# Kernel optimization log

Hardware: AMD Instinct MI355X
Metric: run time of the kernel (lower is better)

## Reference

```python
import jax, jax.numpy as jnp
import numpy as np

B, S, V, D, H, L, FF = 2, 1024, 32000, 512, 8, 4, 2048
DK = D // H
WIN, GLOB = 128, 16
EPS = 1e-5


def setup_inputs() -> dict:
    key = jax.random.key(0)
    ks = jax.random.split(key, 12)
    def rn(k, shape, s=0.02):
        return jax.random.normal(k, shape, jnp.float32) * s
    ln2 = jnp.stack([jnp.ones((L, 2, D)), jnp.zeros((L, 2, D))], axis=2)   # [L, 2 norms, (scale,bias), D]
    ln3 = jnp.stack([jnp.ones((L, 3, D)), jnp.zeros((L, 3, D))], axis=2)   # [L, 3 norms, (scale,bias), D]
    fln = jnp.stack([jnp.ones((D,)), jnp.zeros((D,))], axis=0)             # [(scale,bias), D]
    return {
        "src": jax.random.randint(ks[0], (B, S), 0, V),
        "tgt": jax.random.randint(ks[1], (B, S), 0, V),
        "enc_embed": rn(ks[2], (V, D)),
        "dec_embed": rn(ks[3], (V, D)),
        "enc_attn_w": rn(ks[4], (L, 4, D, D)),   # q,k,v,o projections
        "enc_attn_b": jnp.zeros((L, 4, D)),
        "enc_ln": ln2,
        "enc_ffn_w1": rn(ks[5], (L, D, FF)),
        "enc_ffn_b1": jnp.zeros((L, FF)),
        "enc_ffn_w2": rn(ks[6], (L, FF, D)),
        "enc_ffn_b2": jnp.zeros((L, D)),
        "enc_final_ln": fln,
        "dec_attn_w": rn(ks[7], (L, 8, D, D)),   # self q,k,v,o then cross q,k,v,o
        "dec_attn_b": jnp.zeros((L, 8, D)),
        "dec_ln": ln3,
        "dec_ffn_w1": rn(ks[8], (L, D, FF)),
        "dec_ffn_b1": jnp.zeros((L, FF)),
        "dec_ffn_w2": rn(ks[9], (L, FF, D)),
        "dec_ffn_b2": jnp.zeros((L, D)),
        "dec_final_ln": fln,
        "out_w": rn(ks[10], (D, V)),
        "out_b": jnp.zeros((V,)),
    }


def _ln(x, p):
    m = jnp.mean(x, -1, keepdims=True)
    v = jnp.var(x, -1, keepdims=True)
    return p[0] * (x - m) * jax.lax.rsqrt(v + EPS) + p[1]


def _rope(x):
    # x: [B, H, S, DK]; half-split rotary embedding
    half = DK // 2
    pos = jnp.arange(x.shape[2], dtype=jnp.float32)
    inv = 1.0 / (10000.0 ** (jnp.arange(half, dtype=jnp.float32) / half))
    ang = pos[:, None] * inv[None, :]                   # [S, half]
    c, s = jnp.cos(ang), jnp.sin(ang)
    x1, x2 = x[..., :half], x[..., half:]
    return jnp.concatenate([x1 * c - x2 * s, x1 * s + x2 * c], axis=-1)


def _mask(n, causal):
    # local sliding window + global tokens, optional causal
    i = jnp.arange(n)[:, None]
    j = jnp.arange(n)[None, :]
    allowed = jnp.abs(i - j) <= WIN
    allowed = allowed | (i < GLOB) | (j < GLOB)
    if causal:
        allowed = allowed & (j <= i)
    return allowed


def _attn(q_in, k_in, v_in, w, b, causal):
    # w: [4, D, D] (q,k,v,o), b: [4, D]
    def heads(x, idx):
        y = x @ w[idx] + b[idx]
        return y.reshape(x.shape[0], x.shape[1], H, DK).transpose(0, 2, 1, 3)  # [B,H,S,DK]
    Q, K, Vh = heads(q_in, 0), heads(k_in, 1), heads(v_in, 2)
    Q, K = _rope(Q), _rope(K)
    scores = jnp.einsum('bhqd,bhkd->bhqk', Q, K) / np.sqrt(DK).astype(np.float32)
    scores = jnp.where(_mask(q_in.shape[1], causal)[None, None], scores, -1e9)
    A = jax.nn.softmax(scores, axis=-1)
    o = jnp.einsum('bhqk,bhkd->bhqd', A, Vh).transpose(0, 2, 1, 3).reshape(q_in.shape[0], q_in.shape[1], D)
    return o @ w[3] + b[3]


def _ffn(x, w1, b1, w2, b2):
    return jax.nn.gelu(x @ w1 + b1) @ w2 + b2


def _forward(src, tgt, enc_embed, dec_embed, enc_attn_w, enc_attn_b, enc_ln,
             enc_ffn_w1, enc_ffn_b1, enc_ffn_w2, enc_ffn_b2, enc_final_ln,
             dec_attn_w, dec_attn_b, dec_ln, dec_ffn_w1, dec_ffn_b1,
             dec_ffn_w2, dec_ffn_b2, dec_final_ln, out_w, out_b):
    sqrt_d = np.sqrt(D).astype(np.float32)
    # encoder
    x = enc_embed[src] * sqrt_d
    for l in range(L):
        n = _ln(x, enc_ln[l, 0])
        x = x + _attn(n, n, n, enc_attn_w[l], enc_attn_b[l], False)
        n = _ln(x, enc_ln[l, 1])
        x = x + _ffn(n, enc_ffn_w1[l], enc_ffn_b1[l], enc_ffn_w2[l], enc_ffn_b2[l])
    mem = _ln(x, enc_final_ln)
    # decoder
    y = dec_embed[tgt] * sqrt_d
    for l in range(L):
        n = _ln(y, dec_ln[l, 0])
        y = y + _attn(n, n, n, dec_attn_w[l, :4], dec_attn_b[l, :4], True)
        n = _ln(y, dec_ln[l, 1])
        y = y + _attn(n, mem, mem, dec_attn_w[l, 4:], dec_attn_b[l, 4:], False)
        n = _ln(y, dec_ln[l, 2])
        y = y + _ffn(n, dec_ffn_w1[l], dec_ffn_b1[l], dec_ffn_w2[l], dec_ffn_b2[l])
    y = _ln(y, dec_final_ln)
    return y @ out_w + out_b


def reference(src, tgt, enc_embed, dec_embed, enc_attn_w, enc_attn_b, enc_ln,
              enc_ffn_w1, enc_ffn_b1, enc_ffn_w2, enc_ffn_b2, enc_final_ln,
              dec_attn_w, dec_attn_b, dec_ln, dec_ffn_w1, dec_ffn_b1,
              dec_ffn_w2, dec_ffn_b2, dec_final_ln, out_w, out_b):
    return _forward(src, tgt, enc_embed, dec_embed, enc_attn_w, enc_attn_b, enc_ln,
                    enc_ffn_w1, enc_ffn_b1, enc_ffn_w2, enc_ffn_b2, enc_final_ln,
                    dec_attn_w, dec_attn_b, dec_ln, dec_ffn_w1, dec_ffn_b1,
                    dec_ffn_w2, dec_ffn_b2, dec_final_ln, out_w, out_b)
```

## Files before the change

kernel.cpp:

```cpp
#include <hip/hip_runtime.h>
#include <cstdint>
#include <cstddef>

#define S_LEN 1024
#define DM 512
#define NHEAD 8
#define HDIM 64
#define NLAYER 4
#define FFD 2048
#define VOC 32000
#define WINSZ 128
#define GLOBSZ 16

using half8 = __attribute__((ext_vector_type(8))) _Float16;
using f32x4 = __attribute__((ext_vector_type(4))) float;

static __device__ __forceinline__ f32x4 mfma16(half8 a, half8 b, f32x4 c) {
  return __builtin_amdgcn_mfma_f32_16x16x32_f16(a, b, c, 0, 0, 0);
}

typedef __attribute__((address_space(1))) const void gvoid;
typedef __attribute__((address_space(3))) void lvoid;
static __device__ __forceinline__ void gload16(const void* g, void* l) {
  __builtin_amdgcn_global_load_lds((gvoid*)g, (lvoid*)l, 16, 0, 0);
}
template <int N>
static __device__ __forceinline__ void waitv() {
  asm volatile("s_waitcnt vmcnt(%0)" :: "i"(N) : "memory");
}

__global__ __launch_bounds__(256) void transpose2_k(const float* __restrict__ inA,
                                                    const float* __restrict__ inB,
                                                    _Float16* __restrict__ outA,
                                                    _Float16* __restrict__ outB,
                                                    int R, int C, int splitZ)
{
  __shared__ float t[32][33];
  int z = blockIdx.z;
  const float* ip;
  _Float16* op;
  if (z < splitZ) { ip = inA + (size_t)z * R * C; op = outA + (size_t)z * R * C; }
  else { ip = inB + (size_t)(z - splitZ) * R * C; op = outB + (size_t)(z - splitZ) * R * C; }
  int c0 = blockIdx.x * 32, r0 = blockIdx.y * 32;
  int tx = threadIdx.x & 31, ty = threadIdx.x >> 5;
#pragma unroll
  for (int i = 0; i < 32; i += 8)
    t[ty + i][tx] = ip[(size_t)(r0 + ty + i) * C + c0 + tx];
  __syncthreads();
#pragma unroll
  for (int i = 0; i < 32; i += 8)
    op[(size_t)(c0 + ty + i) * R + r0 + tx] = (_Float16)t[tx][ty + i];
}

__global__ __launch_bounds__(256) void embed2_k(const int* __restrict__ src,
                                                const int* __restrict__ tgt,
                                                const float* __restrict__ enc_embed,
                                                const float* __restrict__ dec_embed,
                                                const float* __restrict__ enc_ln0,
                                                const float* __restrict__ dec_ln0,
                                                float* __restrict__ xbuf,
                                                float* __restrict__ ybuf,
                                                _Float16* __restrict__ nbuf,
                                                _Float16* __restrict__ nbuf2)
{
  int which = blockIdx.y;
  const int* ids = which ? tgt : src;
  const float* emb = which ? dec_embed : enc_embed;
  const float* gamma = which ? dec_ln0 : enc_ln0;
  const float* beta = gamma + 512;
  float* xout = which ? ybuf : xbuf;
  _Float16* nout = which ? nbuf2 : nbuf;

  int row = blockIdx.x * 4 + (threadIdx.x >> 6);
  int lane = threadIdx.x & 63;
  const float* er = emb + (size_t)ids[row] * DM + lane * 8;
  float4 v0 = *(const float4*)er;
  float4 v1 = *(const float4*)(er + 4);
  float vals[8] = {v0.x, v0.y, v0.z, v0.w, v1.x, v1.y, v1.z, v1.w};
  float s = 0.f, ss = 0.f;
#pragma unroll
  for (int j = 0; j < 8; ++j) {
    vals[j] *= 22.627416997969522f;
    s += vals[j]; ss += vals[j] * vals[j];
  }
#pragma unroll
  for (int m = 1; m < 64; m <<= 1) { s += __shfl_xor(s, m); ss += __shfl_xor(ss, m); }
  float mean = s * (1.f / 512.f);
  float var = ss * (1.f / 512.f) - mean * mean;
  float rstd = rsqrtf(var + 1e-5f);
  float* xr = xout + (size_t)row * DM + lane * 8;
  _Float16* orow = nout + (size_t)row * DM + lane * 8;
  const float* gp = gamma + lane * 8;
  const float* bp = beta + lane * 8;
#pragma unroll
  for (int j = 0; j < 8; ++j) {
    xr[j] = vals[j];
    orow[j] = (_Float16)(gp[j] * (vals[j] - mean) * rstd + bp[j]);
  }
}

__global__ __launch_bounds__(256) void ln_k(const float* __restrict__ x,
                                            const float* __restrict__ gamma,
                                            const float* __restrict__ beta,
                                            _Float16* __restrict__ outp)
{
  int row = blockIdx.x * 4 + (threadIdx.x >> 6);
  int lane = threadIdx.x & 63;
  const float* xr = x + (size_t)row * DM + lane * 8;
  float4 v0 = *(const float4*)xr;
  float4 v1 = *(const float4*)(xr + 4);
  float vals[8] = {v0.x, v0.y, v0.z, v0.w, v1.x, v1.y, v1.z, v1.w};
  float s = 0.f, ss = 0.f;
#pragma unroll
  for (int j = 0; j < 8; ++j) { s += vals[j]; ss += vals[j] * vals[j]; }
#pragma unroll
  for (int m = 1; m < 64; m <<= 1) { s += __shfl_xor(s, m); ss += __shfl_xor(ss, m); }
  float mean = s * (1.f / 512.f);
  float var = ss * (1.f / 512.f) - mean * mean;
  float rstd = rsqrtf(var + 1e-5f);
  _Float16* orow = outp + (size_t)row * DM + lane * 8;
  const float* gp = gamma + lane * 8;
  const float* bp = beta + lane * 8;
#pragma unroll
  for (int j = 0; j < 8; ++j)
    orow[j] = (_Float16)(gp[j] * (vals[j] - mean) * rstd + bp[j]);
}

template <int BM, int BN, int EPI, int MODE, bool SWZ = false, bool NT = false, int PIPE = 3>
__global__ __launch_bounds__(256) void gemm_k(const _Float16* __restrict__ A,
                                              const _Float16* __restrict__ B,
                                              const float* __restrict__ bias,
                                              const float* __restrict__ resid,
                                              void* __restrict__ Cout,
                                              _Float16* __restrict__ vtout,
                                              int M, int N, int K)
{
  constexpr bool WIDE = (BN >= 64);
  constexpr int WAVE_M = WIDE ? BM / 4 : BM / 2;
  constexpr int WAVE_N = WIDE ? BN : BN / 2;
  constexpr int FMW = WAVE_M / 16;
  constexpr int FNW = WIDE ? BN / 16 : BN / 32;
  constexpr int LPS = BM / 32 + BN / 32;
  static_assert(MODE == 0 || (WIDE && BN == 64), "rope modes need 64-col waves");

  __shared__ __align__(16) _Float16 As[PIPE][BM * 64];
  __shared__ __align__(16) _Float16 Bs[PIPE][BN * 64];
  const int tid = threadIdx.x;
  const int lane = tid & 63, wid = tid >> 6;
  const int g = lane >> 4, ql = lane & 15;

  int bm, bn;
  if constexpr (SWZ) {
    const int gx = gridDim.x;
    const int nwg = gx * gridDim.y;
    const int orig = blockIdx.y * gx + blockIdx.x;
    const int q = nwg >> 3, r = nwg & 7;
    const int xcd = orig & 7, rest = orig >> 3;
    const int id = (xcd < r ? xcd * (q + 1) : r * (q + 1) + (xcd - r) * q) + rest;
    bm = (id % gx) * BM; bn = (id / gx) * BN;
  } else {
    bm = blockIdx.x * BM; bn = blockIdx.y * BN;
  }
  const int wm = WIDE ? wid * WAVE_M : (wid >> 1) * WAVE_M;
  const int wn = WIDE ? 0 : (wid & 1) * WAVE_N;

  const _Float16* Bp;
  if constexpr (MODE == 2) {
    int srcrow0 = ((bn >> 10) * 8 + 5 + ((bn >> 9) & 1)) * 512 + (bn & 511);
    Bp = B + (size_t)srcrow0 * K;
  } else {
    Bp = B + (size_t)bn * K;
  }

  f32x4 acc[FMW][FNW];
#pragma unroll
  for (int a = 0; a < FMW; ++a)
#pragma unroll
    for (int b = 0; b < FNW; ++b) acc[a][b] = f32x4{0.f, 0.f, 0.f, 0.f};

  auto stage = [&](int buf, int kt) {
#pragma unroll
    for (int r2 = 0; r2 < BM / 32; ++r2) {
      int off = r2 * 4096 + tid * 16;
      int row = off >> 7, slot = (off >> 4) & 7;
      gload16(A + (size_t)(bm + row) * K + kt + ((slot ^ (row & 7)) << 3),
              (char*)&As[buf][0] + r2 * 4096 + wid * 1024);
    }
#pragma unroll
    for (int r2 = 0; r2 < BN / 32; ++r2) {
      int off = r2 * 4096 + tid * 16;
      int row = off >> 7, slot = (off >> 4) & 7;
      gload16(Bp + (size_t)row * K + kt + ((slot ^ (row & 7)) << 3),
              (char*)&Bs[buf][0] + r2 * 4096 + wid * 1024);
    }
  };

  auto compute = [&](int cur) {
#pragma unroll
    for (int kk = 0; kk < 2; ++kk) {
      half8 af[FMW], bf[FNW];
#pragma unroll
      for (int a = 0; a < FMW; ++a) {
        int row = wm + a * 16 + ql;
        af[a] = *(const half8*)((const char*)&As[cur][0] + row * 128 + (((kk * 4 + g) ^ (row & 7)) << 4));
      }
#pragma unroll
      for (int b = 0; b < FNW; ++b) {
        int row = wn + b * 16 + ql;
        bf[b] = *(const half8*)((const char*)&Bs[cur][0] + row * 128 + (((kk * 4 + g) ^ (row & 7)) << 4));
      }
#pragma unroll
      for (int a = 0; a < FMW; ++a)
#pragma unroll
        for (int b = 0; b < FNW; ++b) acc[a][b] = mfma16(af[a], bf[b], acc[a][b]);
    }
  };

  const int nk = K >> 6;
  stage(0, 0);
  stage(1, 64);
  if constexpr (PIPE == 4) stage(2, 128);
  for (int t = 0; t < nk; ++t) {
    if constexpr (PIPE == 3) {
      if (t + 1 < nk) waitv<LPS>(); else waitv<0>();
    } else {
      if (t + 2 < nk) waitv<2 * LPS>();
      else if (t + 1 < nk) waitv<LPS>();
      else waitv<0>();
    }
    __builtin_amdgcn_s_barrier();
    __builtin_amdgcn_sched_barrier(0);
    compute(t % PIPE);
    if (t + PIPE - 1 < nk) stage((t + PIPE - 1) % PIPE, (t + PIPE - 1) << 6);
  }

#pragma unroll
  for (int a = 0; a < FMW; ++a) {
    const int row0 = bm + wm + a * 16 + g * 4;
    float v[FNW][4];
#pragma unroll
    for (int b2 = 0; b2 < FNW; ++b2) {
      int col = bn + wn + b2 * 16 + ql;
      float bv;
      if constexpr (MODE == 2) {
        int bcol = ((col >> 10) * 8 + 5 + ((col >> 9) & 1)) * 512 + (col & 511);
        bv = bias[bcol];
      } else {
        bv = bias[col];
      }
#pragma unroll
      for (int r2 = 0; r2 < 4; ++r2) v[b2][r2] = acc[a][b2][r2] + bv;
    }
    if constexpr (MODE != 0) {
      const int seg = bn >> 9;
      bool dorope = (MODE == 3) || (MODE == 1 && seg < 2) ||
                    (MODE == 2 && ((bn >> 9) & 1) == 0);
      if (dorope) {
        const float scale = (MODE == 3 || (MODE == 1 && seg == 0)) ? 0.125f : 1.0f;
#pragma unroll
        for (int b2 = 0; b2 < 2; ++b2) {
          int d = b2 * 16 + ql;
          float inv = __expf(-(float)d * 0.28782313662425574f);
#pragma unroll
          for (int r2 = 0; r2 < 4; ++r2) {
            float sp = (float)((row0 & 1023) + r2);
            float sn, cs; __sincosf(sp * inv, &sn, &cs);
            float x1 = v[b2][r2], x2 = v[b2 + 2][r2];
            v[b2][r2]     = (x1 * cs - x2 * sn) * scale;
            v[b2 + 2][r2] = (x1 * sn + x2 * cs) * scale;
          }
        }
      }
    }
#pragma unroll
    for (int b2 = 0; b2 < FNW; ++b2) {
      int col = bn + wn + b2 * 16 + ql;
      if constexpr (MODE == 1) {
        if (col < 1024) {
#pragma unroll
          for (int r2 = 0; r2 < 4; ++r2)
            ((_Float16*)Cout)[(size_t)(row0 + r2) * 1024 + col] = (_Float16)v[b2][r2];
        } else {
          int rowidx = ((row0 >> 10) << 9) + (col - 1024);
          union { _Float16 h[4]; uint2 u; } pk;
#pragma unroll
          for (int r2 = 0; r2 < 4; ++r2) pk.h[r2] = (_Float16)v[b2][r2];
          *(uint2*)&vtout[((size_t)rowidx << 10) + (row0 & 1023)] = pk.u;
        }
      } else if constexpr (MODE == 2) {
        if ((col & 1023) < 512) {
#pragma unroll
          for (int r2 = 0; r2 < 4; ++r2)
            ((_Float16*)Cout)[(size_t)(row0 + r2) * 2048 + ((col >> 10) << 9) + (col & 511)] = (_Float16)v[b2][r2];
        } else {
          int rowidx = (col & ~1023) + ((row0 >> 10) << 9) + (col & 511);
          union { _Float16 h[4]; uint2 u; } pk;
#pragma unroll
          for (int r2 = 0; r2 < 4; ++r2) pk.h[r2] = (_Float16)v[b2][r2];
          *(uint2*)&vtout[((size_t)rowidx << 10) + (row0 & 1023)] = pk.u;
        }
      } else {
#pragma unroll
        for (int r2 = 0; r2 < 4; ++r2) {
          float x = v[b2][r2];
          if constexpr (EPI == 1) {
            float u = x;
            x = u / (1.f + __expf(-1.5957691216057308f * (u + 0.044715f * u * u * u)));
          }
          if constexpr (EPI == 2) x += resid[(size_t)(row0 + r2) * N + col];
          if constexpr (EPI == 0 || EPI == 1)
            ((_Float16*)Cout)[(size_t)(row0 + r2) * N + col] = (_Float16)x;
          else if constexpr (NT)
            __builtin_nontemporal_store(x, &((float*)Cout)[(size_t)(row0 + r2) * N + col]);
          else
            ((float*)Cout)[(size_t)(row0 + r2) * N + col] = x;
        }
      }
    }
  }
}

__global__ __launch_bounds__(256) void gemmlg_k(const _Float16* __restrict__ A,
                                                const _Float16* __restrict__ B,
                                                const float* __restrict__ bias,
                                                float* __restrict__ Cout,
                                                int N, int K)
{
  __shared__ __align__(16) _Float16 As[2][128 * 64];
  __shared__ __align__(16) _Float16 Bs[2][128 * 64];
  const int tid = threadIdx.x;
  const int lane = tid & 63, wid = tid >> 6;
  const int g = lane >> 4, ql = lane & 15;

  const int gx = gridDim.x;
  const int nwg = gx * gridDim.y;
  const int orig = blockIdx.y * gx + blockIdx.x;
  const int q = nwg >> 3, r = nwg & 7;
  const int xcd = orig & 7, rest = orig >> 3;
  const int id = (xcd < r ? xcd * (q + 1) : r * (q + 1) + (xcd - r) * q) + rest;
  const int bm = (id % gx) * 128, bn = (id / gx) * 128;
  const int wm = (wid >> 1) * 64, wn = (wid & 1) * 64;

  const _Float16* Bp = B + (size_t)bn * K;

  f32x4 acc[4][4];
#pragma unroll
  for (int a = 0; a < 4; ++a)
#pragma unroll
    for (int b = 0; b < 4; ++b) acc[a][b] = f32x4{0.f, 0.f, 0.f, 0.f};

  auto stage = [&](int buf, int kt) {
#pragma unroll
    for (int r2 = 0; r2 < 4; ++r2) {
      int off = r2 * 4096 + tid * 16;
      int row = off >> 7, slot = (off >> 4) & 7;
      gload16(A + (size_t)(bm + row) * K + kt + ((slot ^ (row & 7)) << 3),
              (char*)&As[buf][0] + r2 * 4096 + wid * 1024);
    }
#pragma unroll
    for (int r2 = 0; r2 < 4; ++r2) {
      int off = r2 * 4096 + tid * 16;
      int row = off >> 7, slot = (off >> 4) & 7;
      gload16(Bp + (size_t)row * K + kt + ((slot ^ (row & 7)) << 3),
              (char*)&Bs[buf][0] + r2 * 4096 + wid * 1024);
    }
  };

  const int nk = K >> 6;
  stage(0, 0);
  for (int t = 0; t < nk; ++t) {
    waitv<0>();
    __builtin_amdgcn_s_barrier();
    __builtin_amdgcn_sched_barrier(0);
    if (t + 1 < nk) stage((t + 1) & 1, (t + 1) << 6);
    const int cur = t & 1;
#pragma unroll
    for (int kk = 0; kk < 2; ++kk) {
      half8 af[4], bf[4];
#pragma unroll
      for (int a = 0; a < 4; ++a) {
        int row = wm + a * 16 + ql;
        af[a] = *(const half8*)((const char*)&As[cur][0] + row * 128 + (((kk * 4 + g) ^ (row & 7)) << 4));
      }
#pragma unroll
      for (int b = 0; b < 4; ++b) {
        int row = wn + b * 16 + ql;
        bf[b] = *(const half8*)((const char*)&Bs[cur][0] + row * 128 + (((kk * 4 + g) ^ (row & 7)) << 4));
      }
#pragma unroll
      for (int a = 0; a < 4; ++a)
#pragma unroll
        for (int b = 0; b < 4; ++b) acc[a][b] = mfma16(af[a], bf[b], acc[a][b]);
    }
  }

#pragma unroll
  for (int a = 0; a < 4; ++a) {
    const int row0 = bm + wm + a * 16 + g * 4;
#pragma unroll
    for (int b2 = 0; b2 < 4; ++b2) {
      int col = bn + wn + b2 * 16 + ql;
      float bv = bias[col];
#pragma unroll
      for (int r2 = 0; r2 < 4; ++r2)
        __builtin_nontemporal_store(acc[a][b2][r2] + bv,
                                    &Cout[(size_t)(row0 + r2) * N + col]);
    }
  }
}

template <bool CAUSAL>
__global__ __launch_bounds__(128) void attn_k(const _Float16* __restrict__ qb, int qs, int qoff,
                                              const _Float16* __restrict__ kb, int ks, int koff,
                                              const _Float16* __restrict__ vt,
                                              _Float16* __restrict__ out)
{
  __shared__ _Float16 plds[2][16 * 40];
  const int bh = blockIdx.y, b = bh >> 3, h = bh & 7;
  const int wid = threadIdx.x >> 6, lane = threadIdx.x & 63;
  const int g = lane >> 4, ql = lane & 15;
  const int q0 = blockIdx.x * 32 + wid * 16;
  const size_t rb = (size_t)b * S_LEN;

  half8 qf0, qf1;
  {
    const _Float16* qp = qb + (rb + q0 + ql) * qs + qoff + h * HDIM + g * 8;
    qf0 = *(const half8*)qp;
    qf1 = *(const half8*)(qp + 32);
  }
  float mrun[4] = {-1e30f, -1e30f, -1e30f, -1e30f};
  float srun[4] = {0.f, 0.f, 0.f, 0.f};
  f32x4 oacc[4];
#pragma unroll
  for (int c = 0; c < 4; ++c) oacc[c] = f32x4{0.f, 0.f, 0.f, 0.f};

  const _Float16* vbase = vt + (((size_t)(b * 512 + h * HDIM)) << 10);
  _Float16* pw = plds[wid];

  auto proc = [&](int k0) {
    const _Float16* kp = kb + (rb + k0 + ql) * ks + koff + h * HDIM + g * 8;
    half8 kf00 = *(const half8*)kp;
    half8 kf01 = *(const half8*)(kp + 32);
    half8 kf10 = *(const half8*)(kp + (size_t)16 * ks);
    half8 kf11 = *(const half8*)(kp + (size_t)16 * ks + 32);

    f32x4 s0 = f32x4{0.f, 0.f, 0.f, 0.f};
    f32x4 s1 = f32x4{0.f, 0.f, 0.f, 0.f};
    s0 = mfma16(qf0, kf00, s0); s0 = mfma16(qf1, kf01, s0);
    s1 = mfma16(qf0, kf10, s1); s1 = mfma16(qf1, kf11, s1);

    float p0[4], p1[4];
#pragma unroll
    for (int r = 0; r < 4; ++r) {
      int i = q0 + 4 * g + r;
      int j0 = k0 + ql, j1 = j0 + 16;
      float a0 = s0[r], a1 = s1[r];
      int d0 = i - j0, d1 = i - j1;
      bool ok0 = (d0 <= WINSZ && d0 >= -WINSZ) || (i < GLOBSZ) || (j0 < GLOBSZ);
      bool ok1 = (d1 <= WINSZ && d1 >= -WINSZ) || (i < GLOBSZ) || (j1 < GLOBSZ);
      if (CAUSAL) { ok0 = ok0 && (j0 <= i); ok1 = ok1 && (j1 <= i); }
      a0 = ok0 ? a0 : -1e9f;
      a1 = ok1 ? a1 : -1e9f;
      float mx = fmaxf(a0, a1);
      mx = fmaxf(mx, __shfl_xor(mx, 1));
      mx = fmaxf(mx, __shfl_xor(mx, 2));
      mx = fmaxf(mx, __shfl_xor(mx, 4));
      mx = fmaxf(mx, __shfl_xor(mx, 8));
      float mnew = fmaxf(mrun[r], mx);
      float alpha = __expf(mrun[r] - mnew);
      float e0 = __expf(a0 - mnew), e1 = __expf(a1 - mnew);
      float ps = e0 + e1;
      ps += __shfl_xor(ps, 1);
      ps += __shfl_xor(ps, 2);
      ps += __shfl_xor(ps, 4);
      ps += __shfl_xor(ps, 8);
      srun[r] = srun[r] * alpha + ps;
      mrun[r] = mnew;
#pragma unroll
      for (int c = 0; c < 4; ++c) oacc[c][r] *= alpha;
      p0[r] = e0; p1[r] = e1;
    }
#pragma unroll
    for (int r = 0; r < 4; ++r) {
      pw[(4 * g + r) * 40 + ql] = (_Float16)p0[r];
      pw[(4 * g + r) * 40 + 16 + ql] = (_Float16)p1[r];
    }
    half8 pa = *(const half8*)&pw[ql * 40 + g * 8];
#pragma unroll
    for (int c = 0; c < 4; ++c) {
      half8 vf = *(const half8*)(vbase + (((size_t)(16 * c + ql)) << 10) + k0 + 8 * g);
      oacc[c] = mfma16(pa, vf, oacc[c]);
    }
  };

  const int kend = CAUSAL ? (q0 + 16) : S_LEN;
  int lo = 0, hi = kend;
  if (q0 >= GLOBSZ) {
    lo = (q0 - WINSZ) & ~31;
    if (lo < 0) lo = 0;
    if (!CAUSAL) {
      int h2 = q0 + 16 + WINSZ;
      hi = (h2 < kend) ? h2 : kend;
    }
  }
  if (lo > 0) proc(0);
  for (int k0 = lo; k0 < hi; k0 += 32) proc(k0);

#pragma unroll
  for (int c = 0; c < 4; ++c)
#pragma unroll
    for (int r = 0; r < 4; ++r) {
      float val = oacc[c][r] / srun[r];
      out[(rb + q0 + 4 * g + r) * DM + h * HDIM + 16 * c + ql] = (_Float16)val;
    }
}

extern "C" void kernel_launch(void* const* d_in, const int* in_sizes, int n_in,
                              void* d_out, int out_size, void* d_ws, size_t ws_size,
                              hipStream_t stream)
{
  const int*   src         = (const int*)d_in[0];
  const int*   tgt         = (const int*)d_in[1];
  const float* enc_embed   = (const float*)d_in[2];
  const float* dec_embed   = (const float*)d_in[3];
  const float* enc_attn_w  = (const float*)d_in[4];
  const float* enc_attn_b  = (const float*)d_in[5];
  const float* enc_ln      = (const float*)d_in[6];
  const float* enc_ffn_w1  = (const float*)d_in[7];
  const float* enc_ffn_b1  = (const float*)d_in[8];
  const float* enc_ffn_w2  = (const float*)d_in[9];
  const float* enc_ffn_b2  = (const float*)d_in[10];
  const float* enc_fln     = (const float*)d_in[11];
  const float* dec_attn_w  = (const float*)d_in[12];
  const float* dec_attn_b  = (const float*)d_in[13];
  const float* dec_ln      = (const float*)d_in[14];
  const float* dec_ffn_w1  = (const float*)d_in[15];
  const float* dec_ffn_b1  = (const float*)d_in[16];
  const float* dec_ffn_w2  = (const float*)d_in[17];
  const float* dec_ffn_b2  = (const float*)d_in[18];
  const float* dec_fln     = (const float*)d_in[19];
  const float* out_w       = (const float*)d_in[20];
  const float* out_b       = (const float*)d_in[21];
  float* logits = (float*)d_out;

  char* wsp = (char*)d_ws;
  size_t off = 0;
  auto alloc = [&](size_t bytes) -> void* {
    void* p = wsp + off;
    off += (bytes + 255) & ~(size_t)255;
    return p;
  };
  _Float16* enc_attn_wt = (_Float16*)alloc((size_t)16 * 512 * 512 * 2);
  _Float16* dec_attn_wt = (_Float16*)alloc((size_t)32 * 512 * 512 * 2);
  _Float16* e_ffn1_wt   = (_Float16*)alloc((size_t)4 * 2048 * 512 * 2);
  _Float16* e_ffn2_wt   = (_Float16*)alloc((size_t)4 * 2048 * 512 * 2);
  _Float16* d_ffn1_wt   = (_Float16*)alloc((size_t)4 * 2048 * 512 * 2);
  _Float16* d_ffn2_wt   = (_Float16*)alloc((size_t)4 * 2048 * 512 * 2);
  _Float16* out_wt      = (_Float16*)alloc((size_t)VOC * 512 * 2);
  float*    xbuf        = (float*)alloc((size_t)2048 * 512 * 4);
  float*    ybuf        = (float*)alloc((size_t)2048 * 512 * 4);
  _Float16* nbuf        = (_Float16*)alloc((size_t)2048 * 512 * 2);
  _Float16* nbuf2       = (_Float16*)alloc((size_t)2048 * 512 * 2);
  _Float16* qkvb        = (_Float16*)alloc((size_t)2048 * 1024 * 2);
  _Float16* aob         = (_Float16*)alloc((size_t)2048 * 512 * 2);
  _Float16* hbuf        = (_Float16*)alloc((size_t)2048 * 2048 * 2);
  _Float16* memb        = (_Float16*)alloc((size_t)2048 * 512 * 2);
  _Float16* cqb         = (_Float16*)alloc((size_t)2048 * 512 * 2);
  _Float16* ckvb        = (_Float16*)alloc((size_t)2048 * 2048 * 2);
  _Float16* vts         = (_Float16*)alloc((size_t)2 * 512 * 1024 * 2);
  _Float16* vtc         = (_Float16*)alloc((size_t)8 * 512 * 1024 * 2);

  transpose2_k<<<dim3(16, 16, 48), 256, 0, stream>>>(enc_attn_w, dec_attn_w,
                                                     enc_attn_wt, dec_attn_wt, 512, 512, 16);
  transpose2_k<<<dim3(64, 16, 8), 256, 0, stream>>>(enc_ffn_w1, dec_ffn_w1,
                                                    e_ffn1_wt, d_ffn1_wt, 512, 2048, 4);
  transpose2_k<<<dim3(16, 64, 8), 256, 0, stream>>>(enc_ffn_w2, dec_ffn_w2,
                                                    e_ffn2_wt, d_ffn2_wt, 2048, 512, 4);
  transpose2_k<<<dim3(1000, 16, 1), 256, 0, stream>>>(out_w, out_w, out_wt, out_wt, 512, VOC, 1);

  embed2_k<<<dim3(512, 2), 256, 0, stream>>>(src, tgt, enc_embed, dec_embed,
                                             enc_ln, dec_ln, xbuf, ybuf, nbuf, nbuf2);

  for (int l = 0; l < NLAYER; ++l) {
    const float* g0 = enc_ln + ((size_t)(l * 2 + 0) * 2 + 0) * 512;
    if (l > 0) ln_k<<<512, 256, 0, stream>>>(xbuf, g0, g0 + 512, nbuf);
    gemm_k<64, 64, 0, 1, true><<<dim3(32, 24), 256, 0, stream>>>(
        nbuf, enc_attn_wt + (size_t)l * 4 * 262144,
        enc_attn_b + (size_t)l * 4 * 512, nullptr, qkvb, vts, 2048, 1536, 512);
    attn_k<false><<<dim3(32, 16), 128, 0, stream>>>(qkvb, 1024, 0, qkvb, 1024, 512, vts, aob);
    gemm_k<64, 32, 2, 0><<<dim3(32, 16), 256, 0, stream>>>(
        aob, enc_attn_wt + (size_t)(l * 4 + 3) * 262144,
        enc_attn_b + (size_t)(l * 4 + 3) * 512, xbuf, xbuf, nullptr, 2048, 512, 512);
    const float* g1 = enc_ln + ((size_t)(l * 2 + 1) * 2 + 0) * 512;
    ln_k<<<512, 256, 0, stream>>>(xbuf, g1, g1 + 512, nbuf);
    gemm_k<64, 64, 1, 0, true><<<dim3(32, 32), 256, 0, stream>>>(
        nbuf, e_ffn1_wt + (size_t)l * 2048 * 512,
        enc_ffn_b1 + (size_t)l * 2048, nullptr, hbuf, nullptr, 2048, 2048, 512);
    gemm_k<64, 32, 2, 0, false, false, 4><<<dim3(32, 16), 256, 0, stream>>>(
        hbuf, e_ffn2_wt + (size_t)l * 512 * 2048,
        enc_ffn_b2 + (size_t)l * 512, xbuf, xbuf, nullptr, 2048, 512, 2048);
  }
  ln_k<<<512, 256, 0, stream>>>(xbuf, enc_fln, enc_fln + 512, memb);

  gemm_k<64, 64, 0, 2, true><<<dim3(32, 64), 256, 0, stream>>>(
      memb, dec_attn_wt, dec_attn_b, nullptr, ckvb, vtc, 2048, 4096, 512);

  for (int l = 0; l < NLAYER; ++l) {
    const float* g0 = dec_ln + ((size_t)(l * 3 + 0) * 2 + 0) * 512;
    const _Float16* dn = (l == 0) ? nbuf2 : nbuf;
    if (l > 0) ln_k<<<512, 256, 0, stream>>>(ybuf, g0, g0 + 512, nbuf);
    gemm_k<64, 64, 0, 1, true><<<dim3(32, 24), 256, 0, stream>>>(
        dn, dec_attn_wt + (size_t)l * 8 * 262144,
        dec_attn_b + (size_t)l * 8 * 512, nullptr, qkvb, vts, 2048, 1536, 512);
    attn_k<true><<<dim3(32, 16), 128, 0, stream>>>(qkvb, 1024, 0, qkvb, 1024, 512, vts, aob);
    gemm_k<64, 32, 2, 0><<<dim3(32, 16), 256, 0, stream>>>(
        aob, dec_attn_wt + (size_t)(l * 8 + 3) * 262144,
        dec_attn_b + (size_t)(l * 8 + 3) * 512, ybuf, ybuf, nullptr, 2048, 512, 512);
    const float* g1 = dec_ln + ((size_t)(l * 3 + 1) * 2 + 0) * 512;
    ln_k<<<512, 256, 0, stream>>>(ybuf, g1, g1 + 512, nbuf);
    gemm_k<64, 64, 0, 3><<<dim3(32, 8), 256, 0, stream>>>(
        nbuf, dec_attn_wt + (size_t)(l * 8 + 4) * 262144,
        dec_attn_b + (size_t)(l * 8 + 4) * 512, nullptr, cqb, nullptr, 2048, 512, 512);
    attn_k<false><<<dim3(32, 16), 128, 0, stream>>>(cqb, 512, 0, ckvb, 2048, l * 512,
                                                    vtc + ((size_t)l << 20), aob);
    gemm_k<64, 32, 2, 0><<<dim3(32, 16), 256, 0, stream>>>(
        aob, dec_attn_wt + (size_t)(l * 8 + 7) * 262144,
        dec_attn_b + (size_t)(l * 8 + 7) * 512, ybuf, ybuf, nullptr, 2048, 512, 512);
    const float* g2 = dec_ln + ((size_t)(l * 3 + 2) * 2 + 0) * 512;
    ln_k<<<512, 256, 0, stream>>>(ybuf, g2, g2 + 512, nbuf);
    gemm_k<64, 64, 1, 0, true><<<dim3(32, 32), 256, 0, stream>>>(
        nbuf, d_ffn1_wt + (size_t)l * 2048 * 512,
        dec_ffn_b1 + (size_t)l * 2048, nullptr, hbuf, nullptr, 2048, 2048, 512);
    gemm_k<64, 32, 2, 0, false, false, 4><<<dim3(32, 16), 256, 0, stream>>>(
        hbuf, d_ffn2_wt + (size_t)l * 512 * 2048,
        dec_ffn_b2 + (size_t)l * 512, ybuf, ybuf, nullptr, 2048, 512, 2048);
  }

  ln_k<<<512, 256, 0, stream>>>(ybuf, dec_fln, dec_fln + 512, nbuf);
  gemmlg_k<<<dim3(16, 250), 256, 0, stream>>>(nbuf, out_wt, out_b, logits, VOC, 512);
}
```

Baseline: 970.1 us.

## Fuse residual GEMMs with following LayerNorm via grid-wide atomic barrier

Adds a gemmresln_k kernel that does the output-projection or FFN2 GEMM with bias and residual add, then waits on a global atomic counter until all 512 blocks finish before applying LayerNorm to 4 rows per block. This removes all standalone ln_k launches and their extra pass over the residual stream. The 4-stage pipeline variant for the K=2048 FFN2 GEMM is dropped in favor of the 3-stage one. The grid barrier assumes all 512 blocks are co-resident, which risks a deadlock if occupancy is insufficient, and adds spin-wait cost.

After: 2.974 ms. 3.07x slower.

```diff
diff --git a/kernel.cpp b/kernel.cpp
--- a/kernel.cpp
+++ b/kernel.cpp
@@ -99,34 +99,7 @@
   }
 }
 
-__global__ __launch_bounds__(256) void ln_k(const float* __restrict__ x,
-                                            const float* __restrict__ gamma,
-                                            const float* __restrict__ beta,
-                                            _Float16* __restrict__ outp)
-{
-  int row = blockIdx.x * 4 + (threadIdx.x >> 6);
-  int lane = threadIdx.x & 63;
-  const float* xr = x + (size_t)row * DM + lane * 8;
-  float4 v0 = *(const float4*)xr;
-  float4 v1 = *(const float4*)(xr + 4);
-  float vals[8] = {v0.x, v0.y, v0.z, v0.w, v1.x, v1.y, v1.z, v1.w};
-  float s = 0.f, ss = 0.f;
-#pragma unroll
-  for (int j = 0; j < 8; ++j) { s += vals[j]; ss += vals[j] * vals[j]; }
-#pragma unroll
-  for (int m = 1; m < 64; m <<= 1) { s += __shfl_xor(s, m); ss += __shfl_xor(ss, m); }
-  float mean = s * (1.f / 512.f);
-  float var = ss * (1.f / 512.f) - mean * mean;
-  float rstd = rsqrtf(var + 1e-5f);
-  _Float16* orow = outp + (size_t)row * DM + lane * 8;
-  const float* gp = gamma + lane * 8;
-  const float* bp = beta + lane * 8;
-#pragma unroll
-  for (int j = 0; j < 8; ++j)
-    orow[j] = (_Float16)(gp[j] * (vals[j] - mean) * rstd + bp[j]);
-}
-
-template <int BM, int BN, int EPI, int MODE, bool SWZ = false, bool NT = false, int PIPE = 3>
+template <int BM, int BN, int EPI, int MODE, bool SWZ = false, bool NT = false>
 __global__ __launch_bounds__(256) void gemm_k(const _Float16* __restrict__ A,
                                               const _Float16* __restrict__ B,
                                               const float* __restrict__ bias,
@@ -143,8 +116,8 @@
   constexpr int LPS = BM / 32 + BN / 32;
   static_assert(MODE == 0 || (WIDE && BN == 64), "rope modes need 64-col waves");
 
-  __shared__ __align__(16) _Float16 As[PIPE][BM * 64];
-  __shared__ __align__(16) _Float16 Bs[PIPE][BN * 64];
+  __shared__ __align__(16) _Float16 As[3][BM * 64];
+  __shared__ __align__(16) _Float16 Bs[3][BN * 64];
   const int tid = threadIdx.x;
   const int lane = tid & 63, wid = tid >> 6;
   const int g = lane >> 4, ql = lane & 15;
@@ -219,19 +192,12 @@
   const int nk = K >> 6;
   stage(0, 0);
   stage(1, 64);
-  if constexpr (PIPE == 4) stage(2, 128);
   for (int t = 0; t < nk; ++t) {
-    if constexpr (PIPE == 3) {
-      if (t + 1 < nk) waitv<LPS>(); else waitv<0>();
-    } else {
-      if (t + 2 < nk) waitv<2 * LPS>();
-      else if (t + 1 < nk) waitv<LPS>();
-      else waitv<0>();
-    }
+    if (t + 1 < nk) waitv<LPS>(); else waitv<0>();
     __builtin_amdgcn_s_barrier();
     __builtin_amdgcn_sched_barrier(0);
-    compute(t % PIPE);
-    if (t + PIPE - 1 < nk) stage((t + PIPE - 1) % PIPE, (t + PIPE - 1) << 6);
+    compute(t % 3);
+    if (t + 2 < nk) stage((t + 2) % 3, (t + 2) << 6);
   }
 
 #pragma unroll
@@ -317,6 +283,120 @@
         }
       }
     }
+  }
+}
+
+__global__ __launch_bounds__(256) void gemmresln_k(const _Float16* __restrict__ A,
+                                                   const _Float16* __restrict__ B,
+                                                   const float* __restrict__ bias,
+                                                   float* __restrict__ resid,
+                                                   const float* __restrict__ gamma,
+                                                   const float* __restrict__ beta,
+                                                   _Float16* __restrict__ lnout,
+                                                   unsigned* __restrict__ cnt,
+                                                   int K)
+{
+  __shared__ __align__(16) _Float16 As[3][64 * 64];
+  __shared__ __align__(16) _Float16 Bs[3][32 * 64];
+  const int tid = threadIdx.x;
+  const int lane = tid & 63, wid = tid >> 6;
+  const int g = lane >> 4, ql = lane & 15;
+  const int bm = blockIdx.x * 64, bn = blockIdx.y * 32;
+  const int wm = (wid >> 1) * 32, wn = (wid & 1) * 16;
+
+  const _Float16* Bp = B + (size_t)bn * K;
+
+  f32x4 acc[2];
+  acc[0] = f32x4{0.f, 0.f, 0.f, 0.f};
+  acc[1] = f32x4{0.f, 0.f, 0.f, 0.f};
+
+  auto stage = [&](int buf, int kt) {
+#pragma unroll
+    for (int r2 = 0; r2 < 2; ++r2) {
+      int off = r2 * 4096 + tid * 16;
+      int row = off >> 7, slot = (off >> 4) & 7;
+      gload16(A + (size_t)(bm + row) * K + kt + ((slot ^ (row & 7)) << 3),
+              (char*)&As[buf][0] + r2 * 4096 + wid * 1024);
+    }
+    {
+      int off = tid * 16;
+      int row = off >> 7, slot = (off >> 4) & 7;
+      gload16(Bp + (size_t)row * K + kt + ((slot ^ (row & 7)) << 3),
+              (char*)&Bs[buf][0] + wid * 1024);
+    }
+  };
+
+  auto compute = [&](int cur) {
+#pragma unroll
+    for (int kk = 0; kk < 2; ++kk) {
+      half8 af[2], bf;
+#pragma unroll
+      for (int a = 0; a < 2; ++a) {
+        int row = wm + a * 16 + ql;
+        af[a] = *(const half8*)((const char*)&As[cur][0] + row * 128 + (((kk * 4 + g) ^ (row & 7)) << 4));
+      }
+      {
+        int row = wn + ql;
+        bf = *(const half8*)((const char*)&Bs[cur][0] + row * 128 + (((kk * 4 + g) ^ (row & 7)) << 4));
+      }
+      acc[0] = mfma16(af[0], bf, acc[0]);
+      acc[1] = mfma16(af[1], bf, acc[1]);
+    }
+  };
+
+  const int nk = K >> 6;
+  stage(0, 0);
+  stage(1, 64);
+  for (int t = 0; t < nk; ++t) {
+    if (t + 1 < nk) waitv<3>(); else waitv<0>();
+    __builtin_amdgcn_s_barrier();
+    __builtin_amdgcn_sched_barrier(0);
+    compute(t % 3);
+    if (t + 2 < nk) stage((t + 2) % 3, (t + 2) << 6);
+  }
+
+#pragma unroll
+  for (int a = 0; a < 2; ++a) {
+    const int row0 = bm + wm + a * 16 + g * 4;
+    const int col = bn + wn + ql;
+    const float bv = bias[col];
+#pragma unroll
+    for (int r2 = 0; r2 < 4; ++r2) {
+      float x = acc[a][r2] + bv + resid[(size_t)(row0 + r2) * 512 + col];
+      resid[(size_t)(row0 + r2) * 512 + col] = x;
+    }
+  }
+
+  __threadfence();
+  __syncthreads();
+  if (tid == 0) {
+    atomicAdd(cnt, 1u);
+    while (atomicAdd(cnt, 0u) < 512u) __builtin_amdgcn_s_sleep(8);
+  }
+  __syncthreads();
+  __threadfence();
+
+  {
+    const int flat = blockIdx.y * gridDim.x + blockIdx.x;
+    const int row = flat * 4 + (tid >> 6);
+    const float* xr = resid + (size_t)row * DM + lane * 8;
+    float4 v0 = *(const float4*)xr;
+    float4 v1 = *(const float4*)(xr + 4);
+    float vals[8] = {v0.x, v0.y, v0.z, v0.w, v1.x, v1.y, v1.z, v1.w};
+    float s = 0.f, ss = 0.f;
+#pragma unroll
+    for (int j = 0; j < 8; ++j) { s += vals[j]; ss += vals[j] * vals[j]; }
+#pragma unroll
+    for (int m = 1; m < 64; m <<= 1) { s += __shfl_xor(s, m); ss += __shfl_xor(ss, m); }
+    float mean = s * (1.f / 512.f);
+    float var = ss * (1.f / 512.f) - mean * mean;
+    float rstd = rsqrtf(var + 1e-5f);
+    _Float16* orow = lnout + (size_t)row * DM + lane * 8;
+    const float* gp = gamma + lane * 8;
+    const float* bp = beta + lane * 8;
+#pragma unroll
+    for (int j = 0; j < 8; ++j)
+      orow[j] = (_Float16)(gp[j] * (vals[j] - mean) * rstd + bp[j]);
   }
 }
 
@@ -569,6 +649,12 @@
   _Float16* ckvb        = (_Float16*)alloc((size_t)2048 * 2048 * 2);
   _Float16* vts         = (_Float16*)alloc((size_t)2 * 512 * 1024 * 2);
   _Float16* vtc         = (_Float16*)alloc((size_t)8 * 512 * 1024 * 2);
+  unsigned* syncb       = (unsigned*)alloc((size_t)24 * 64);
+
+  hipMemsetAsync(syncb, 0, 24 * 64, stream);
+
+  int sc = 0;
+  auto cntp = [&]() { return syncb + (sc++) * 16; };
 
   transpose2_k<<<dim3(16, 16, 48), 256, 0, stream>>>(enc_attn_w, dec_attn_w,
                                                      enc_attn_wt, dec_attn_wt, 512, 512, 16);
@@ -582,60 +668,54 @@
                                              enc_ln, dec_ln, xbuf, ybuf, nbuf, nbuf2);
 
   for (int l = 0; l < NLAYER; ++l) {
-    const float* g0 = enc_ln + ((size_t)(l * 2 + 0) * 2 + 0) * 512;
-    if (l > 0) ln_k<<<512, 256, 0, stream>>>(xbuf, g0, g0 + 512, nbuf);
     gemm_k<64, 64, 0, 1, true><<<dim3(32, 24), 256, 0, stream>>>(
         nbuf, enc_attn_wt + (size_t)l * 4 * 262144,
         enc_attn_b + (size_t)l * 4 * 512, nullptr, qkvb, vts, 2048, 1536, 512);
     attn_k<false><<<dim3(32, 16), 128, 0, stream>>>(qkvb, 1024, 0, qkvb, 1024, 512, vts, aob);
-    gemm_k<64, 32, 2, 0><<<dim3(32, 16), 256, 0, stream>>>(
+    const float* g1 = enc_ln + ((size_t)(l * 2 + 1) * 2 + 0) * 512;
+    gemmresln_k<<<dim3(32, 16), 256, 0, stream>>>(
         aob, enc_attn_wt + (size_t)(l * 4 + 3) * 262144,
-        enc_attn_b + (size_t)(l * 4 + 3) * 512, xbuf, xbuf, nullptr, 2048, 512, 512);
-    const float* g1 = enc_ln + ((size_t)(l * 2 + 1) * 2 + 0) * 512;
-    ln_k<<<512, 256, 0, stream>>>(xbuf, g1, g1 + 512, nbuf);
+        enc_attn_b + (size_t)(l * 4 + 3) * 512, xbuf, g1, g1 + 512, nbuf, cntp(), 512);
     gemm_k<64, 64, 1, 0, true><<<dim3(32, 32), 256, 0, stream>>>(
         nbuf, e_ffn1_wt + (size_t)l * 2048 * 512,
         enc_ffn_b1 + (size_t)l * 2048, nullptr, hbuf, nullptr, 2048, 2048, 512);
-    gemm_k<64, 32, 2, 0, false, false, 4><<<dim3(32, 16), 256, 0, stream>>>(
+    const float* gn = (l < 3) ? (enc_ln + ((size_t)((l + 1) * 2 + 0) * 2 + 0) * 512) : enc_fln;
+    _Float16* lnout = (l < 3) ? nbuf : memb;
+    gemmresln_k<<<dim3(32, 16), 256, 0, stream>>>(
         hbuf, e_ffn2_wt + (size_t)l * 512 * 2048,
-        enc_ffn_b2 + (size_t)l * 512, xbuf, xbuf, nullptr, 2048, 512, 2048);
-  }
-  ln_k<<<512, 256, 0, stream>>>(xbuf, enc_fln, enc_fln + 512, memb);
+        enc_ffn_b2 + (size_t)l * 512, xbuf, gn, gn + 512, lnout, cntp(), 2048);
+  }
 
   gemm_k<64, 64, 0, 2, true><<<dim3(32, 64), 256, 0, stream>>>(
       memb, dec_attn_wt, dec_attn_b, nullptr, ckvb, vtc, 2048, 4096, 512);
 
   for (int l = 0; l < NLAYER; ++l) {
-    const float* g0 = dec_ln + ((size_t)(l * 3 + 0) * 2 + 0) * 512;
     const _Float16* dn = (l == 0) ? nbuf2 : nbuf;
-    if (l > 0) ln_k<<<512, 256, 0, stream>>>(ybuf, g0, g0 + 512, nbuf);
     gemm_k<64, 64, 0, 1, true><<<dim3(32, 24), 256, 0, stream>>>(
         dn, dec_attn_wt + (size_t)l * 8 * 262144,
         dec_attn_b + (size_t)l * 8 * 512, nullptr, qkvb, vts, 2048, 1536, 512);
     attn_k<true><<<dim3(32, 16), 128, 0, stream>>>(qkvb, 1024, 0, qkvb, 1024, 512, vts, aob);
-    gemm_k<64, 32, 2, 0><<<dim3(32, 16), 256, 0, stream>>>(
+    const float* g1 = dec_ln + ((size_t)(l * 3 + 1) * 2 + 0) * 512;
+    gemmresln_k<<<dim3(32, 16), 256, 0, stream>>>(
         aob, dec_attn_wt + (size_t)(l * 8 + 3) * 262144,
-        dec_attn_b + (size_t)(l * 8 + 3) * 512, ybuf, ybuf, nullptr, 2048, 512, 512);
-    const float* g1 = dec_ln + ((size_t)(l * 3 + 1) * 2 + 0) * 512;
-    ln_k<<<512, 256, 0, stream>>>(ybuf, g1, g1 + 512, nbuf);
+        dec_attn_b + (size_t)(l * 8 + 3) * 512, ybuf, g1, g1 + 512, nbuf, cntp(), 512);
     gemm_k<64, 64, 0, 3><<<dim3(32, 8), 256, 0, stream>>>(
         nbuf, dec_attn_wt + (size_t)(l * 8 + 4) * 262144,
         dec_attn_b + (size_t)(l * 8 + 4) * 512, nullptr, cqb, nullptr, 2048, 512, 512);
     attn_k<false><<<dim3(32, 16), 128, 0, stream>>>(cqb, 512, 0, ckvb, 2048, l * 512,
                                                     vtc + ((size_t)l << 20), aob);
-    gemm_k<64, 32, 2, 0><<<dim3(32, 16), 256, 0, stream>>>(
+    const float* g2 = dec_ln + ((size_t)(l * 3 + 2) * 2 + 0) * 512;
+    gemmresln_k<<<dim3(32, 16), 256, 0, stream>>>(
         aob, dec_attn_wt + (size_t)(l * 8 + 7) * 262144,
-        dec_attn_b + (size_t)(l * 8 + 7) * 512, ybuf, ybuf, nullptr, 2048, 512, 512);
-    const float* g2 = dec_ln + ((size_t)(l * 3 + 2) * 2 + 0) * 512;
-    ln_k<<<512, 256, 0, stream>>>(ybuf, g2, g2 + 512, nbuf);
+        dec_attn_b + (size_t)(l * 8 + 7) * 512, ybuf, g2, g2 + 512, nbuf, cntp(), 512);
     gemm_k<64, 64, 1, 0, true><<<dim3(32, 32), 256, 0, stream>>>(
         nbuf, d_ffn1_wt + (size_t)l * 2048 * 512,
         dec_ffn_b1 + (size_t)l * 2048, nullptr, hbuf, nullptr, 2048, 2048, 512);
-    gemm_k<64, 32, 2, 0, false, false, 4><<<dim3(32, 16), 256, 0, stream>>>(
+    const float* gn = (l < 3) ? (dec_ln + ((size_t)((l + 1) * 3 + 0) * 2 + 0) * 512) : dec_fln;
+    gemmresln_k<<<dim3(32, 16), 256, 0, stream>>>(
         hbuf, d_ffn2_wt + (size_t)l * 512 * 2048,
-        dec_ffn_b2 + (size_t)l * 512, ybuf, ybuf, nullptr, 2048, 512, 2048);
-  }
-
-  ln_k<<<512, 256, 0, stream>>>(ybuf, dec_fln, dec_fln + 512, nbuf);
+        dec_ffn_b2 + (size_t)l * 512, ybuf, gn, gn + 512, nbuf, cntp(), 2048);
+  }
+
   gemmlg_k<<<dim3(16, 250), 256, 0, stream>>>(nbuf, out_wt, out_b, logits, VOC, 512);
 }
```
